# Performance work log

Measured on AMD Instinct MI355X. Metric: run time of the kernel, lower is better.

## Reference

```python
import jax, jax.numpy as jnp
import numpy as np

B, S, D, H, K = 2, 2048, 1024, 16, 16


def setup_inputs() -> dict:
    key = jax.random.key(0)
    ks = jax.random.split(key, 8)
    s = 0.02
    def w(k, shape):
        return s * jax.random.normal(k, shape, jnp.float32)
    return {
        "x": jax.random.normal(ks[0], (B, S, D), jnp.float32),
        "Wq": w(ks[1], (D, D)), "bq": jnp.zeros((D,), jnp.float32),
        "Wk": w(ks[2], (D, D)), "bk": jnp.zeros((D,), jnp.float32),
        "Wv": w(ks[3], (D, D)), "bv": jnp.zeros((D,), jnp.float32),
        "Wo": w(ks[4], (D, D)), "bo": jnp.zeros((D,), jnp.float32),
        "Ws1": w(ks[5], (D, D // 2)), "bs1": jnp.zeros((D // 2,), jnp.float32),
        "Ws2": w(ks[6], (D // 2, 1)), "bs2": jnp.zeros((1,), jnp.float32),
    }


def reference(x, Wq, bq, Wk, bk, Wv, bv, Wo, bo, Ws1, bs1, Ws2, bs2):
    Bx, Sx, Dx = x.shape
    Dh = Dx // H
    # QKV projections -> [B, H, S, Dh]
    q = (x @ Wq + bq).reshape(Bx, Sx, H, Dh).transpose(0, 2, 1, 3)
    k = (x @ Wk + bk).reshape(Bx, Sx, H, Dh).transpose(0, 2, 1, 3)
    v = (x @ Wv + bv).reshape(Bx, Sx, H, Dh).transpose(0, 2, 1, 3)
    scores = jnp.einsum('bhqd,bhkd->bhqk', q, k) / np.float32(np.sqrt(Dh))
    # Lightning-indexer importance: [B, S]; identical across heads, so compute once.
    imp = jax.nn.sigmoid(jax.nn.relu(x @ Ws1 + bs1) @ Ws2 + bs2)[..., 0]
    _, idx = jax.lax.top_k(imp, K)  # [B, K]
    sel = jnp.zeros((Bx, Sx), bool).at[jnp.arange(Bx)[:, None], idx].set(True)
    # sparse mask: position (i, j) kept if row i OR column j is a top-k token
    m2 = sel[:, :, None] | sel[:, None, :]  # [B, S, S]
    masked = jnp.where(m2[:, None, :, :], scores, -jnp.inf)
    w = jax.nn.softmax(masked, axis=-1)
    att = jnp.einsum('bhqk,bhkd->bhqd', w, v).transpose(0, 2, 1, 3).reshape(Bx, Sx, Dx)
    return att @ Wo + bo
```

## Files before the change

kernel.cpp:

```cpp
#include <hip/hip_runtime.h>
#include <math.h>

constexpr int Bb = 2, Ss = 2048, Dd = 1024, Hh = 16, Kk = 16;
constexpr float DELTA = 0.02f;

typedef __bf16 bf16x8 __attribute__((ext_vector_type(8)));
typedef __bf16 bf16x4 __attribute__((ext_vector_type(4)));
typedef float  f32x4  __attribute__((ext_vector_type(4)));

__device__ __forceinline__ void gld_lds16(const void* g, void* l) {
    __builtin_amdgcn_global_load_lds(
        (const __attribute__((address_space(1))) unsigned int*)g,
        (__attribute__((address_space(3))) unsigned int*)l, 16, 0, 0);
}

__global__ void __launch_bounds__(256) prep_kernel(
    const float* __restrict__ x, __bf16* __restrict__ xb,
    __bf16* __restrict__ xbT,
    float* __restrict__ imp, float* __restrict__ hbuf,
    float* __restrict__ qkvsel, int* __restrict__ ccount,
    const float* __restrict__ Ws1, __bf16* __restrict__ W1Th,
    const float* __restrict__ bv, const float* __restrict__ bo,
    float* __restrict__ Y, float* __restrict__ zbuf,
    float* __restrict__ obuf)
{
    __shared__ float tile[32][33];
    const int bid = blockIdx.x;
    const int t   = threadIdx.x;

    if (bid < 1024) {
        int i = bid * 256 + t;
        float4 z4 = {0.f, 0.f, 0.f, 0.f};
        if (i < 131072) ((float4*)Y)[i] = z4;
        if (i < 16384)  ((float4*)hbuf)[i] = z4;
        if (i < 24576)  ((float4*)qkvsel)[i] = z4;
        if (i < 8192)   ((float4*)zbuf)[i] = ((const float4*)bv)[i & 255];
        if (i < 8192)   ((float4*)obuf)[i] = ((const float4*)bo)[i & 255];
        if (i < 1024)   ((float4*)imp)[i] = z4;
        if (i < Bb)     ccount[i] = 0;
        return;
    }
    if (bid < 5120) {
        int tid = bid - 1024;
        int b   = tid >> 11;
        int rem = tid & 2047;
        int rt  = rem >> 5;
        int ct  = rem & 31;
        int tx = t & 31, ty = t >> 5;
        const float* xp = x + (size_t)b * Ss * Dd;
        __bf16* xbp = xb + (size_t)b * Ss * Dd;
        #pragma unroll
        for (int i2 = 0; i2 < 32; i2 += 8) {
            float v = xp[(size_t)(rt * 32 + ty + i2) * 1024 + ct * 32 + tx];
            tile[ty + i2][tx] = v;
            xbp[(size_t)(rt * 32 + ty + i2) * 1024 + ct * 32 + tx] = (__bf16)v;
        }
        __syncthreads();
        __bf16* xT = xbT + (size_t)b * Dd * Ss;
        #pragma unroll
        for (int i2 = 0; i2 < 32; i2 += 8)
            xT[(size_t)(ct * 32 + ty + i2) * 2048 + rt * 32 + tx] = (__bf16)tile[tx][ty + i2];
        return;
    }
    {
        int tid = bid - 5120;
        int n0 = (tid & 15) * 32;
        int k0 = (tid >> 4) * 32;
        int tx = t & 31, ty = t >> 5;
        #pragma unroll
        for (int i2 = 0; i2 < 32; i2 += 8)
            tile[ty + i2][tx] = Ws1[(size_t)(k0 + ty + i2) * 512 + n0 + tx];
        __syncthreads();
        #pragma unroll
        for (int i2 = 0; i2 < 32; i2 += 8)
            W1Th[(size_t)(n0 + ty + i2) * 1024 + k0 + tx] = (__bf16)tile[tx][ty + i2];
    }
}

__global__ void __launch_bounds__(256) gemm_ind(
    const __bf16* __restrict__ xb, const __bf16* __restrict__ W1Th,
    const float* __restrict__ bs1, const float* __restrict__ Ws2,
    float* __restrict__ imp)
{
    __shared__ __bf16 As[64 * 64];
    __shared__ __bf16 Bs[128 * 64];

    const int cb   = blockIdx.x;
    const int bm   = blockIdx.y * 64;
    const int t    = threadIdx.x;
    const int wave = t >> 6;
    const int lane = t & 63;
    const int wm   = (wave & 1) * 32;
    const int wn   = (wave >> 1) * 64;
    const int fr   = lane & 15;
    const int fq   = lane >> 4;
    const int K    = Dd;

    const __bf16* BT = W1Th + (size_t)cb * 128 * 1024;

    f32x4 acc[2][4] = {};

    for (int k0 = 0; k0 < K; k0 += 64) {
        #pragma unroll
        for (int l = 0; l < 2; ++l) {
            int c = l * 256 + t;
            int row = c >> 3, seg = (c & 7) ^ (row & 7);
            gld_lds16(xb + (size_t)(bm + row) * K + k0 + seg * 8,
                      As + (size_t)(l * 256 + wave * 64) * 8);
        }
        #pragma unroll
        for (int l = 0; l < 4; ++l) {
            int c = l * 256 + t;
            int row = c >> 3, seg = (c & 7) ^ (row & 7);
            gld_lds16(BT + (size_t)row * K + k0 + seg * 8,
                      Bs + (size_t)(l * 256 + wave * 64) * 8);
        }
        __syncthreads();
        #pragma unroll
        for (int s = 0; s < 2; ++s) {
            bf16x8 af[2], bf[4];
            #pragma unroll
            for (int i = 0; i < 2; ++i) {
                int row = wm + i * 16 + fr;
                af[i] = *(const bf16x8*)(As + row * 64 + (((s * 4 + fq) ^ (row & 7)) * 8));
            }
            #pragma unroll
            for (int j = 0; j < 4; ++j) {
                int row = wn + j * 16 + fr;
                bf[j] = *(const bf16x8*)(Bs + row * 64 + (((s * 4 + fq) ^ (row & 7)) * 8));
            }
            #pragma unroll
            for (int i = 0; i < 2; ++i)
                #pragma unroll
                for (int j = 0; j < 4; ++j)
                    acc[i][j] = __builtin_amdgcn_mfma_f32_16x16x32_bf16(af[i], bf[j], acc[i][j], 0, 0, 0);
        }
        __syncthreads();
    }

    const int cr = (lane >> 4) * 4;
    const int cc = lane & 15;
    float bb[4], w2[4];
    #pragma unroll
    for (int j = 0; j < 4; ++j) {
        int col = cb * 128 + wn + j * 16 + cc;
        bb[j] = bs1[col];
        w2[j] = Ws2[col];
    }
    #pragma unroll
    for (int i = 0; i < 2; ++i) {
        #pragma unroll
        for (int r = 0; r < 4; ++r) {
            float vsum = 0.f;
            #pragma unroll
            for (int j = 0; j < 4; ++j)
                vsum += fmaxf(acc[i][j][r] + bb[j], 0.f) * w2[j];
            #pragma unroll
            for (int off = 8; off > 0; off >>= 1)
                vsum += __shfl_xor(vsum, off, 16);
            if (cc == 0)
                atomicAdd(imp + (bm + wm + i * 16 + cr + r), vsum);
        }
    }
}

__global__ void __launch_bounds__(256) topk_fast(
    const float* __restrict__ imp, int* __restrict__ cand_idx,
    int* __restrict__ ccount)
{
    __shared__ float vals[2048];
    __shared__ float thr_s;
    __shared__ int   cnt_s;
    const int b = blockIdx.x;
    const int t = threadIdx.x;

    #pragma unroll
    for (int e = 0; e < 8; ++e)
        vals[t + 256 * e] = imp[b * Ss + t + 256 * e];
    __syncthreads();

    if (t < 64) {
        const int base = t * 32;
        for (int it = 0; it < Kk; ++it) {
            float best = -1e30f; int bidx = 0x7fffffff;
            #pragma unroll 8
            for (int j = 0; j < 32; ++j) {
                float v = vals[base + j];
                if (v > best) { best = v; bidx = base + j; }
            }
            #pragma unroll
            for (int off = 32; off > 0; off >>= 1) {
                float ov = __shfl_xor(best, off, 64);
                int   oi = __shfl_xor(bidx, off, 64);
                if (ov > best || (ov == best && oi < bidx)) { best = ov; bidx = oi; }
            }
            if (t == 0) {
                cand_idx[b * 64 + it] = bidx;
                vals[bidx] = -1e30f;
                if (it == Kk - 1) { thr_s = best - DELTA; cnt_s = Kk; }
            }
        }
    }
    __syncthreads();

    float thr = thr_s;
    #pragma unroll
    for (int e = 0; e < 8; ++e) {
        if (vals[t + 256 * e] > thr) {
            int p = atomicAdd(&cnt_s, 1);
            if (p < 64) cand_idx[b * 64 + p] = t + 256 * e;
        }
    }
    __syncthreads();
    if (t == 0) ccount[b] = min(cnt_s, 64);
}

__global__ void __launch_bounds__(256) rescore_h(
    const float* __restrict__ x, const float* __restrict__ Ws1,
    const int* __restrict__ cand_idx, const int* __restrict__ ccount,
    float* __restrict__ hbuf)
{
    const int c = blockIdx.x, kc = blockIdx.y, b = blockIdx.z;
    if (c >= ccount[b]) return;
    const int row = cand_idx[b * 64 + c];
    const int t = threadIdx.x;
    const int k0 = kc * 64;

    __shared__ float xs[64];
    if (t < 16)
        ((float4*)xs)[t] = ((const float4*)(x + ((size_t)(b * Ss + row)) * Dd + k0))[t];
    __syncthreads();

    float a0 = 0.f, a1 = 0.f;
    const float* W = Ws1 + (size_t)k0 * 512;
    #pragma unroll 16
    for (int kk = 0; kk < 64; ++kk) {
        float xv = xs[kk];
        a0 = fmaf(xv, W[kk * 512 + t], a0);
        a1 = fmaf(xv, W[kk * 512 + t + 256], a1);
    }
    float* hb = hbuf + ((size_t)(b * 64 + c)) * 512;
    atomicAdd(hb + t, a0);
    atomicAdd(hb + t + 256, a1);
}

__global__ void __launch_bounds__(256) rescore_fin_sel(
    const float* __restrict__ hbuf, const float* __restrict__ bs1,
    const float* __restrict__ Ws2, const int* __restrict__ cand_idx,
    const int* __restrict__ ccount, int* __restrict__ sel_idx)
{
    const int b = blockIdx.x;
    const int t = threadIdx.x;
    __shared__ float czv[64];
    __shared__ int   cidx[64];
    const int cntb = ccount[b];

    {
        const int cc = t >> 2, part = t & 3;
        const float* hb = hbuf + ((size_t)(b * 64 + cc)) * 512;
        float z = 0.f;
        const int j0 = part * 128;
        for (int j = j0; j < j0 + 128; ++j)
            z += fmaxf(hb[j] + bs1[j], 0.f) * Ws2[j];
        z += __shfl_xor(z, 1, 4);
        z += __shfl_xor(z, 2, 4);
        if (part == 0) { czv[cc] = z; cidx[cc] = cand_idx[b * 64 + cc]; }
    }
    __syncthreads();

    if (t < 64) {
        float val = (t < cntb) ? czv[t] : -1e30f;
        int   row = (t < cntb) ? cidx[t] : 0x7fffffff;
        for (int it = 0; it < Kk; ++it) {
            float bv = val; int br = row;
            #pragma unroll
            for (int off = 1; off < 64; off <<= 1) {
                float ov = __shfl_xor(bv, off, 64);
                int   orw = __shfl_xor(br, off, 64);
                if (ov > bv || (ov == bv && orw < br)) { bv = ov; br = orw; }
            }
            if (row == br) val = -1e30f;
            if (t == 0) sel_idx[b * Kk + it] = br;
        }
    }
}

__global__ void __launch_bounds__(256) proj_sel(
    const float* __restrict__ x,
    const float* __restrict__ Wq, const float* __restrict__ Wk,
    const float* __restrict__ Wv,
    const int* __restrict__ sel_idx, float* __restrict__ qkvsel)
{
    const int cx = blockIdx.x;
    const int m  = blockIdx.y;
    const int kc = blockIdx.z;
    const int t  = threadIdx.x;
    __shared__ int   sj[32];
    __shared__ float xs[32][128];

    if (t < 32) sj[t] = sel_idx[t];
    __syncthreads();

    const int k0 = kc * 128;
    #pragma unroll
    for (int l = 0; l < 4; ++l) {
        int c = l * 256 + t;
        int r = c >> 5, kq = c & 31;
        int b = r >> 4;
        float4 v = *(const float4*)(x + ((size_t)(b * Ss + sj[r])) * Dd + k0 + kq * 4);
        *(float4*)&xs[r][kq * 4] = v;
    }
    __syncthreads();

    const float* W = (m == 0) ? Wq : (m == 1) ? Wk : Wv;
    const int col = cx * 128 + (t & 127);
    const int rh  = t >> 7;
    float acc[16] = {};
    #pragma unroll 4
    for (int kk = 0; kk < 128; ++kk) {
        float wv = W[(size_t)(k0 + kk) * 1024 + col];
        #pragma unroll
        for (int r = 0; r < 16; ++r)
            acc[r] = fmaf(xs[rh * 16 + r][kk], wv, acc[r]);
    }
    #pragma unroll
    for (int r = 0; r < 16; ++r)
        atomicAdd(qkvsel + (size_t)(m * 32 + rh * 16 + r) * 1024 + col, acc[r]);
}

__global__ void __launch_bounds__(256) build_cdvo(
    const float* __restrict__ Wq, const float* __restrict__ Wk,
    const float* __restrict__ Wo,
    const float* __restrict__ bq, const float* __restrict__ bk,
    const float* __restrict__ bv,
    const float* __restrict__ qkvsel, float* __restrict__ beta,
    __bf16* __restrict__ ET, __bf16* __restrict__ VoT)
{
    const int nx = blockIdx.x;
    const int h  = blockIdx.y;
    const int b  = blockIdx.z;
    const int t  = threadIdx.x;
    __shared__ float qs[16][64], ks[16][64], vs[16][64];
    __shared__ float wt[128][65];

    #pragma unroll
    for (int l = 0; l < 12; ++l) {
        int c = l * 256 + t;
        int mat = c >> 10, rem = c & 1023;
        int row = rem >> 6, d = rem & 63;
        const float* bias = (mat == 0) ? bq : (mat == 1) ? bk : bv;
        float v = qkvsel[(size_t)(mat * 32 + b * 16 + row) * 1024 + h * 64 + d]
                + bias[h * 64 + d];
        if (mat == 0) qs[row][d] = v;
        else if (mat == 1) ks[row][d] = v;
        else vs[row][d] = v;
    }
    __syncthreads();

    if (nx == 0 && t < 16) {
        float a = 0.f;
        #pragma unroll 8
        for (int d = 0; d < 64; ++d) a = fmaf(bq[h * 64 + d], ks[t][d], a);
        beta[b * 256 + h * 16 + t] = a;
    }

    const int nl = t & 127;
    const int n  = nx * 128 + nl;
    const int sg = t >> 7;

    #pragma unroll
    for (int l = 0; l < 8; ++l) {
        int c = l * 256 + t;
        int rn = c >> 4, c4 = c & 15;
        float4 v = *(const float4*)(Wq + (size_t)(nx * 128 + rn) * 1024 + h * 64 + c4 * 4);
        wt[rn][c4 * 4 + 0] = v.x; wt[rn][c4 * 4 + 1] = v.y;
        wt[rn][c4 * 4 + 2] = v.z; wt[rn][c4 * 4 + 3] = v.w;
    }
    __syncthreads();
    {
        float acc[8] = {};
        #pragma unroll 8
        for (int d = 0; d < 64; ++d) {
            float wv = wt[nl][d];
            #pragma unroll
            for (int s = 0; s < 8; ++s)
                acc[s] = fmaf(wv, ks[sg * 8 + s][d], acc[s]);
        }
        #pragma unroll
        for (int s = 0; s < 8; ++s)
            ET[(size_t)(b * 512 + h * 16 + sg * 8 + s) * 1024 + n] = (__bf16)acc[s];
    }
    __syncthreads();

    #pragma unroll
    for (int l = 0; l < 8; ++l) {
        int c = l * 256 + t;
        int rn = c >> 4, c4 = c & 15;
        float4 v = *(const float4*)(Wk + (size_t)(nx * 128 + rn) * 1024 + h * 64 + c4 * 4);
        wt[rn][c4 * 4 + 0] = v.x; wt[rn][c4 * 4 + 1] = v.y;
        wt[rn][c4 * 4 + 2] = v.z; wt[rn][c4 * 4 + 3] = v.w;
    }
    __syncthreads();
    {
        float acc[8] = {};
        #pragma unroll 8
        for (int d = 0; d < 64; ++d) {
            float wv = wt[nl][d];
            #pragma unroll
            for (int s = 0; s < 8; ++s)
                acc[s] = fmaf(wv, qs[sg * 8 + s][d], acc[s]);
        }
        #pragma unroll
        for (int s = 0; s < 8; ++s)
            ET[(size_t)(b * 512 + 256 + h * 16 + sg * 8 + s) * 1024 + n] = (__bf16)acc[s];
    }

    {
        float acc[8] = {};
        #pragma unroll 8
        for (int d = 0; d < 64; ++d) {
            float wv = Wo[(size_t)(h * 64 + d) * 1024 + n];
            #pragma unroll
            for (int s = 0; s < 8; ++s)
                acc[s] = fmaf(wv, vs[sg * 8 + s][d], acc[s]);
        }
        #pragma unroll
        for (int s = 0; s < 8; ++s)
            VoT[((size_t)b * 1024 + n) * 256 + h * 16 + sg * 8 + s] = (__bf16)acc[s];
    }
}

__global__ void __launch_bounds__(256) gemm_scores(
    const __bf16* __restrict__ xb, const __bf16* __restrict__ ET,
    float* __restrict__ Ssp, float* __restrict__ SdT)
{
    __shared__ __bf16 As[64 * 64];
    __shared__ __bf16 Bs[128 * 64];

    const int b    = blockIdx.z;
    const int bn   = blockIdx.x * 128;
    const int bm   = blockIdx.y * 64;
    const int t    = threadIdx.x;
    const int wave = t >> 6;
    const int lane = t & 63;
    const int wm   = (wave & 1) * 32;
    const int wn   = (wave >> 1) * 64;
    const int fr   = lane & 15;
    const int fq   = lane >> 4;
    const int K    = Dd;

    const __bf16* A  = xb + (size_t)b * Ss * Dd;
    const __bf16* BT = ET + (size_t)b * 512 * 1024 + (size_t)bn * 1024;

    f32x4 acc[2][4] = {};

    for (int k0 = 0; k0 < K; k0 += 64) {
        #pragma unroll
        for (int l = 0; l < 2; ++l) {
            int c = l * 256 + t;
            int row = c >> 3, seg = (c & 7) ^ (row & 7);
            gld_lds16(A + (size_t)(bm + row) * K + k0 + seg * 8,
                      As + (size_t)(l * 256 + wave * 64) * 8);
        }
        #pragma unroll
        for (int l = 0; l < 4; ++l) {
            int c = l * 256 + t;
            int row = c >> 3, seg = (c & 7) ^ (row & 7);
            gld_lds16(BT + (size_t)row * K + k0 + seg * 8,
                      Bs + (size_t)(l * 256 + wave * 64) * 8);
        }
        __syncthreads();
        #pragma unroll
        for (int s = 0; s < 2; ++s) {
            bf16x8 af[2], bf[4];
            #pragma unroll
            for (int i = 0; i < 2; ++i) {
                int row = wm + i * 16 + fr;
                af[i] = *(const bf16x8*)(As + row * 64 + (((s * 4 + fq) ^ (row & 7)) * 8));
            }
            #pragma unroll
            for (int j = 0; j < 4; ++j) {
                int row = wn + j * 16 + fr;
                bf[j] = *(const bf16x8*)(Bs + row * 64 + (((s * 4 + fq) ^ (row & 7)) * 8));
            }
            #pragma unroll
            for (int i = 0; i < 2; ++i)
                #pragma unroll
                for (int j = 0; j < 4; ++j)
                    acc[i][j] = __builtin_amdgcn_mfma_f32_16x16x32_bf16(af[i], bf[j], acc[i][j], 0, 0, 0);
        }
        __syncthreads();
    }

    const int cr = (lane >> 4) * 4;
    const int cc = lane & 15;
    #pragma unroll
    for (int j = 0; j < 4; ++j) {
        int col = bn + wn + j * 16 + cc;
        #pragma unroll
        for (int i = 0; i < 2; ++i) {
            int row0 = bm + wm + i * 16 + cr;
            if (col < 256) {
                #pragma unroll
                for (int r = 0; r < 4; ++r)
                    Ssp[((size_t)b * 2048 + row0 + r) * 256 + col] = acc[i][j][r];
            } else {
                *(f32x4*)(SdT + ((size_t)b * 256 + col - 256) * 2048 + row0) = acc[i][j];
            }
        }
    }
}

__global__ void __launch_bounds__(256) sm_all(
    const float* __restrict__ Ssp, const float* __restrict__ beta,
    __bf16* __restrict__ Wsp,
    const float* __restrict__ SdT, __bf16* __restrict__ WdT)
{
    __shared__ float red[256];
    const int b = blockIdx.y;
    const int t = threadIdx.x;

    if (blockIdx.x < 512) {
        const int r = blockIdx.x * 4 + (t >> 6);
        const int l = t & 63;
        float4 v  = *(const float4*)(Ssp + ((size_t)b * 2048 + r) * 256 + l * 4);
        float4 bt = *(const float4*)(beta + b * 256 + l * 4);
        float e0 = __expf((v.x + bt.x) * 0.125f);
        float e1 = __expf((v.y + bt.y) * 0.125f);
        float e2 = __expf((v.z + bt.z) * 0.125f);
        float e3 = __expf((v.w + bt.w) * 0.125f);
        float ps = e0 + e1 + e2 + e3;
        ps += __shfl_xor(ps, 1, 64);
        ps += __shfl_xor(ps, 2, 64);
        float inv = 1.f / ps;
        bf16x4 w = { (__bf16)(e0 * inv), (__bf16)(e1 * inv),
                     (__bf16)(e2 * inv), (__bf16)(e3 * inv) };
        *(bf16x4*)(Wsp + ((size_t)b * 2048 + r) * 256 + l * 4) = w;
    } else {
        const int cx = blockIdx.x - 512;
        const float* Sp = SdT + ((size_t)b * 256 + cx) * 2048;
        float4 v0 = *(const float4*)(Sp + t * 8);
        float4 v1 = *(const float4*)(Sp + t * 8 + 4);
        float e[8];
        e[0] = __expf(v0.x * 0.125f); e[1] = __expf(v0.y * 0.125f);
        e[2] = __expf(v0.z * 0.125f); e[3] = __expf(v0.w * 0.125f);
        e[4] = __expf(v1.x * 0.125f); e[5] = __expf(v1.y * 0.125f);
        e[6] = __expf(v1.z * 0.125f); e[7] = __expf(v1.w * 0.125f);
        float ps = 0.f;
        #pragma unroll
        for (int i = 0; i < 8; ++i) ps += e[i];
        red[t] = ps;
        __syncthreads();
        for (int off = 128; off > 0; off >>= 1) {
            if (t < off) red[t] += red[t + off];
            __syncthreads();
        }
        float inv = 1.f / red[0];
        bf16x8 w;
        #pragma unroll
        for (int i = 0; i < 8; ++i) w[i] = (__bf16)(e[i] * inv);
        *(bf16x8*)(WdT + ((size_t)b * 256 + cx) * 2048 + t * 8) = w;
    }
}

__device__ __forceinline__ void gemm_bt_body(
    __bf16* As, __bf16* Bs,
    const __bf16* __restrict__ A, const __bf16* __restrict__ BT,
    const float* __restrict__ bias, float* __restrict__ C,
    int N, int K, int bm, int bn, int kc, int kchunks, int t)
{
    const int wave = t >> 6;
    const int lane = t & 63;
    const int wm   = (wave & 1) * 32;
    const int wn   = (wave >> 1) * 64;
    const int fr   = lane & 15;
    const int fq   = lane >> 4;
    const int KC   = K / kchunks;
    const int kend = (kc + 1) * KC;

    f32x4 acc[2][4] = {};

    for (int k0 = kc * KC; k0 < kend; k0 += 64) {
        #pragma unroll
        for (int l = 0; l < 2; ++l) {
            int c = l * 256 + t;
            int row = c >> 3, seg = (c & 7) ^ (row & 7);
            gld_lds16(A + (size_t)(bm + row) * K + k0 + seg * 8,
                      As + (size_t)(l * 256 + wave * 64) * 8);
        }
        #pragma unroll
        for (int l = 0; l < 4; ++l) {
            int c = l * 256 + t;
            int row = c >> 3, seg = (c & 7) ^ (row & 7);
            gld_lds16(BT + (size_t)(bn + row) * K + k0 + seg * 8,
                      Bs + (size_t)(l * 256 + wave * 64) * 8);
        }
        __syncthreads();
        #pragma unroll
        for (int s = 0; s < 2; ++s) {
            bf16x8 af[2], bf[4];
            #pragma unroll
            for (int i = 0; i < 2; ++i) {
                int row = wm + i * 16 + fr;
                af[i] = *(const bf16x8*)(As + row * 64 + (((s * 4 + fq) ^ (row & 7)) * 8));
            }
            #pragma unroll
            for (int j = 0; j < 4; ++j) {
                int row = wn + j * 16 + fr;
                bf[j] = *(const bf16x8*)(Bs + row * 64 + (((s * 4 + fq) ^ (row & 7)) * 8));
            }
            #pragma unroll
            for (int i = 0; i < 2; ++i)
                #pragma unroll
                for (int j = 0; j < 4; ++j)
                    acc[i][j] = __builtin_amdgcn_mfma_f32_16x16x32_bf16(af[i], bf[j], acc[i][j], 0, 0, 0);
        }
        __syncthreads();
    }

    const int cr = (lane >> 4) * 4;
    const int cc = lane & 15;
    #pragma unroll
    for (int j = 0; j < 4; ++j) {
        int col = bn + wn + j * 16 + cc;
        if (kchunks == 1) {
            float bb = bias ? bias[col] : 0.f;
            #pragma unroll
            for (int i = 0; i < 2; ++i)
                #pragma unroll
                for (int r = 0; r < 4; ++r)
                    C[(size_t)(bm + wm + i * 16 + cr + r) * N + col] = acc[i][j][r] + bb;
        } else {
            #pragma unroll
            for (int i = 0; i < 2; ++i)
                #pragma unroll
                for (int r = 0; r < 4; ++r)
                    atomicAdd(C + (size_t)(bm + wm + i * 16 + cr + r) * N + col, acc[i][j][r]);
        }
    }
}

__global__ void __launch_bounds__(256) gemm_bt2x(
    const __bf16* __restrict__ Wsp, const __bf16* __restrict__ VoT,
    const float* __restrict__ bo, float* __restrict__ out,
    const __bf16* __restrict__ WdT, const __bf16* __restrict__ xbT,
    float* __restrict__ Y)
{
    __shared__ __bf16 As[64 * 64];
    __shared__ __bf16 Bs[128 * 64];
    const int t = threadIdx.x;
    int id = blockIdx.x;
    if (id < 512) {
        int bx = id & 7, by = (id >> 3) & 31, bz = id >> 8;
        gemm_bt_body(As, Bs,
                     Wsp + (size_t)bz * 2048 * 256, VoT + (size_t)bz * 1024 * 256,
                     bo, out + (size_t)bz * 2048 * 1024,
                     1024, 256, by * 64, bx * 128, 0, 1, t);
    } else {
        id -= 512;
        int bx = id & 7, by = (id >> 3) & 3, z = id >> 5;
        int batch = z >> 1, kc = z & 1;
        gemm_bt_body(As, Bs,
                     WdT + (size_t)batch * 256 * 2048, xbT + (size_t)batch * 1024 * 2048,
                     nullptr, Y + (size_t)batch * 256 * 1024,
                     1024, 2048, by * 64, bx * 128, kc, 2, t);
    }
}

__global__ void __launch_bounds__(256) dense_z2(
    const float* __restrict__ Y, const float* __restrict__ Wv,
    float* __restrict__ zbuf)
{
    const int h = blockIdx.x, kc = blockIdx.y, b = blockIdx.z;
    const int t = threadIdx.x;
    __shared__ float Ys[16][128];
    const int k0 = kc * 128;
    #pragma unroll
    for (int l = 0; l < 2; ++l) {
        int c = l * 256 + t;
        int row = c >> 5, c4 = c & 31;
        *(float4*)&Ys[row][c4 * 4] =
            *(const float4*)(Y + ((size_t)(b * 256 + h * 16 + row)) * 1024 + k0 + c4 * 4);
    }
    __syncthreads();
    const int d = t & 63, tg = t >> 6;
    float acc[4] = {};
    #pragma unroll 8
    for (int kk = 0; kk < 128; ++kk) {
        float wv = Wv[(size_t)(k0 + kk) * 1024 + h * 64 + d];
        #pragma unroll
        for (int tt = 0; tt < 4; ++tt)
            acc[tt] = fmaf(Ys[tg * 4 + tt][kk], wv, acc[tt]);
    }
    #pragma unroll
    for (int tt = 0; tt < 4; ++tt)
        atomicAdd(zbuf + ((size_t)(b * 16 + tg * 4 + tt)) * 1024 + h * 64 + d, acc[tt]);
}

__global__ void __launch_bounds__(256) dense_out2(
    const float* __restrict__ zbuf, const float* __restrict__ Wo,
    float* __restrict__ obuf)
{
    const int nt = blockIdx.x, kc = blockIdx.y, b = blockIdx.z;
    const int t = threadIdx.x;
    __shared__ float zs[16][128];
    const int k0 = kc * 128;
    #pragma unroll
    for (int l = 0; l < 2; ++l) {
        int c = l * 256 + t;
        int row = c >> 5, c4 = c & 31;
        *(float4*)&zs[row][c4 * 4] =
            *(const float4*)(zbuf + ((size_t)(b * 16 + row)) * 1024 + k0 + c4 * 4);
    }
    __syncthreads();
    const int n = nt * 64 + (t & 63), tg = t >> 6;
    float acc[4] = {};
    #pragma unroll 8
    for (int kk = 0; kk < 128; ++kk) {
        float wv = Wo[(size_t)(k0 + kk) * 1024 + n];
        #pragma unroll
        for (int tt = 0; tt < 4; ++tt)
            acc[tt] = fmaf(zs[tg * 4 + tt][kk], wv, acc[tt]);
    }
    #pragma unroll
    for (int tt = 0; tt < 4; ++tt)
        atomicAdd(obuf + ((size_t)(b * 16 + tg * 4 + tt)) * 1024 + n, acc[tt]);
}

__global__ void __launch_bounds__(256) scatter_out(
    const float* __restrict__ obuf, const int* __restrict__ sel_idx,
    float* __restrict__ out)
{
    const int bid = blockIdx.x;
    const int b = bid >> 4, row = bid & 15;
    const int i = sel_idx[b * 16 + row];
    f32x4 v = *(const f32x4*)(obuf + ((size_t)(b * 16 + row)) * 1024 + threadIdx.x * 4);
    *(f32x4*)(out + ((size_t)(b * 2048 + i)) * 1024 + threadIdx.x * 4) = v;
}

extern "C" void kernel_launch(void* const* d_in, const int* in_sizes, int n_in,
                              void* d_out, int out_size, void* d_ws, size_t ws_size,
                              hipStream_t stream)
{
    const float* x   = (const float*)d_in[0];
    const float* Wq  = (const float*)d_in[1];
    const float* bq  = (const float*)d_in[2];
    const float* Wk  = (const float*)d_in[3];
    const float* bk  = (const float*)d_in[4];
    const float* Wv  = (const float*)d_in[5];
    const float* bv  = (const float*)d_in[6];
    const float* Wo  = (const float*)d_in[7];
    const float* bo  = (const float*)d_in[8];
    const float* Ws1 = (const float*)d_in[9];
    const float* bs1 = (const float*)d_in[10];
    const float* Ws2 = (const float*)d_in[11];
    float* out = (float*)d_out;

    const size_t MSD = (size_t)Bb * Ss * Dd;

    char* p = (char*)d_ws;
    __bf16* xb    = (__bf16*)p; p += MSD * sizeof(__bf16);
    __bf16* xbT   = (__bf16*)p; p += MSD * sizeof(__bf16);
    __bf16* W1Th  = (__bf16*)p; p += (size_t)512 * 1024 * sizeof(__bf16);
    __bf16* ET    = (__bf16*)p; p += (size_t)2 * 512 * 1024 * sizeof(__bf16);
    __bf16* VoT   = (__bf16*)p; p += (size_t)2 * 1024 * 256 * sizeof(__bf16);
    __bf16* Wsp   = (__bf16*)p; p += (size_t)2 * 2048 * 256 * sizeof(__bf16);
    __bf16* WdT   = (__bf16*)p; p += (size_t)2 * 256 * 2048 * sizeof(__bf16);
    float* Ssp    = (float*)p; p += (size_t)2 * 2048 * 256 * sizeof(float);
    float* SdT    = (float*)p; p += (size_t)2 * 256 * 2048 * sizeof(float);
    float* Y      = (float*)p; p += (size_t)2 * 256 * 1024 * sizeof(float);
    float* zbuf   = (float*)p; p += (size_t)2 * 16 * 1024 * sizeof(float);
    float* obuf   = (float*)p; p += (size_t)2 * 16 * 1024 * sizeof(float);
    float* imp    = (float*)p; p += (size_t)Bb * Ss * sizeof(float);
    float* hbuf   = (float*)p; p += (size_t)Bb * 64 * 512 * sizeof(float);
    float* qkvsel = (float*)p; p += (size_t)3 * 32 * 1024 * sizeof(float);
    float* beta   = (float*)p; p += (size_t)2 * 256 * sizeof(float);
    int* sel_idx  = (int*)p; p += (size_t)Bb * Kk * sizeof(int);
    int* cand_idx = (int*)p; p += (size_t)Bb * 64 * sizeof(int);
    int* ccount   = (int*)p; p += Bb * sizeof(int);

    prep_kernel<<<dim3(5632), 256, 0, stream>>>(
        x, xb, xbT, imp, hbuf, qkvsel, ccount, Ws1, W1Th,
        bv, bo, Y, zbuf, obuf);
    gemm_ind<<<dim3(4, 64), 256, 0, stream>>>(xb, W1Th, bs1, Ws2, imp);
    topk_fast<<<dim3(Bb), 256, 0, stream>>>(imp, cand_idx, ccount);
    rescore_h<<<dim3(64, 16, Bb), 256, 0, stream>>>(x, Ws1, cand_idx, ccount, hbuf);
    rescore_fin_sel<<<dim3(Bb), 256, 0, stream>>>(
        hbuf, bs1, Ws2, cand_idx, ccount, sel_idx);
    proj_sel<<<dim3(8, 3, 8), 256, 0, stream>>>(x, Wq, Wk, Wv, sel_idx, qkvsel);
    build_cdvo<<<dim3(8, 16, 2), 256, 0, stream>>>(
        Wq, Wk, Wo, bq, bk, bv, qkvsel, beta, ET, VoT);
    gemm_scores<<<dim3(4, 32, 2), 256, 0, stream>>>(xb, ET, Ssp, SdT);
    sm_all<<<dim3(768, 2), 256, 0, stream>>>(Ssp, beta, Wsp, SdT, WdT);
    gemm_bt2x<<<dim3(640), 256, 0, stream>>>(Wsp, VoT, bo, out, WdT, xbT, Y);
    dense_z2<<<dim3(16, 8, 2), 256, 0, stream>>>(Y, Wv, zbuf);
    dense_out2<<<dim3(16, 8, 2), 256, 0, stream>>>(zbuf, Wo, obuf);
    scatter_out<<<dim3(32), 256, 0, stream>>>(obuf, sel_idx, out);
}
```

Measured before the change: 256.8 us.

## Fuse sparse softmax into score GEMM epilogue and scatter into output GEMV

The per-head 16-column softmax for the selected-key scores now runs inside the gemm_scores epilogue, using 16-lane shuffles, and writes bf16 weights directly. This removes the fp32 Ssp intermediate and its read-back. The dense_out2 kernel now atomically adds straight into the selected output rows. Those rows are first reset to the bias in the gemm_bt2x epilogue, which removes the obuf buffer, its initialisation and the scatter_out launch. In exchange the epilogue does uncoalesced scalar bf16 stores and a 16-way compare per output element.

```diff
diff --git a/kernel.cpp b/kernel.cpp
--- a/kernel.cpp
+++ b/kernel.cpp
@@ -20,9 +20,8 @@
     float* __restrict__ imp, float* __restrict__ hbuf,
     float* __restrict__ qkvsel, int* __restrict__ ccount,
     const float* __restrict__ Ws1, __bf16* __restrict__ W1Th,
-    const float* __restrict__ bv, const float* __restrict__ bo,
-    float* __restrict__ Y, float* __restrict__ zbuf,
-    float* __restrict__ obuf)
+    const float* __restrict__ bv,
+    float* __restrict__ Y, float* __restrict__ zbuf)
 {
     __shared__ float tile[32][33];
     const int bid = blockIdx.x;
@@ -35,7 +34,6 @@
         if (i < 16384)  ((float4*)hbuf)[i] = z4;
         if (i < 24576)  ((float4*)qkvsel)[i] = z4;
         if (i < 8192)   ((float4*)zbuf)[i] = ((const float4*)bv)[i & 255];
-        if (i < 8192)   ((float4*)obuf)[i] = ((const float4*)bo)[i & 255];
         if (i < 1024)   ((float4*)imp)[i] = z4;
         if (i < Bb)     ccount[i] = 0;
         return;
@@ -432,7 +430,8 @@
 
 __global__ void __launch_bounds__(256) gemm_scores(
     const __bf16* __restrict__ xb, const __bf16* __restrict__ ET,
-    float* __restrict__ Ssp, float* __restrict__ SdT)
+    const float* __restrict__ beta, __bf16* __restrict__ Wsp,
+    float* __restrict__ SdT)
 {
     __shared__ __bf16 As[64 * 64];
     __shared__ __bf16 Bs[128 * 64];
@@ -494,80 +493,75 @@
 
     const int cr = (lane >> 4) * 4;
     const int cc = lane & 15;
-    #pragma unroll
-    for (int j = 0; j < 4; ++j) {
-        int col = bn + wn + j * 16 + cc;
-        #pragma unroll
-        for (int i = 0; i < 2; ++i) {
-            int row0 = bm + wm + i * 16 + cr;
-            if (col < 256) {
+    if (bn < 256) {
+        #pragma unroll
+        for (int j = 0; j < 4; ++j) {
+            int col = bn + wn + j * 16 + cc;
+            float bt = beta[b * 256 + col];
+            #pragma unroll
+            for (int i = 0; i < 2; ++i) {
                 #pragma unroll
-                for (int r = 0; r < 4; ++r)
-                    Ssp[((size_t)b * 2048 + row0 + r) * 256 + col] = acc[i][j][r];
-            } else {
+                for (int r = 0; r < 4; ++r) {
+                    float e = __expf((acc[i][j][r] + bt) * 0.125f);
+                    float ps = e;
+                    ps += __shfl_xor(ps, 1, 16);
+                    ps += __shfl_xor(ps, 2, 16);
+                    ps += __shfl_xor(ps, 4, 16);
+                    ps += __shfl_xor(ps, 8, 16);
+                    int row = bm + wm + i * 16 + cr + r;
+                    Wsp[((size_t)b * 2048 + row) * 256 + col] = (__bf16)(e / ps);
+                }
+            }
+        }
+    } else {
+        #pragma unroll
+        for (int j = 0; j < 4; ++j) {
+            int col = bn + wn + j * 16 + cc;
+            #pragma unroll
+            for (int i = 0; i < 2; ++i) {
+                int row0 = bm + wm + i * 16 + cr;
                 *(f32x4*)(SdT + ((size_t)b * 256 + col - 256) * 2048 + row0) = acc[i][j];
             }
         }
     }
 }
 
-__global__ void __launch_bounds__(256) sm_all(
-    const float* __restrict__ Ssp, const float* __restrict__ beta,
-    __bf16* __restrict__ Wsp,
+__global__ void __launch_bounds__(256) sm_dense(
     const float* __restrict__ SdT, __bf16* __restrict__ WdT)
 {
+    const int b = blockIdx.y, cx = blockIdx.x;
+    const int t = threadIdx.x;
     __shared__ float red[256];
-    const int b = blockIdx.y;
-    const int t = threadIdx.x;
-
-    if (blockIdx.x < 512) {
-        const int r = blockIdx.x * 4 + (t >> 6);
-        const int l = t & 63;
-        float4 v  = *(const float4*)(Ssp + ((size_t)b * 2048 + r) * 256 + l * 4);
-        float4 bt = *(const float4*)(beta + b * 256 + l * 4);
-        float e0 = __expf((v.x + bt.x) * 0.125f);
-        float e1 = __expf((v.y + bt.y) * 0.125f);
-        float e2 = __expf((v.z + bt.z) * 0.125f);
-        float e3 = __expf((v.w + bt.w) * 0.125f);
-        float ps = e0 + e1 + e2 + e3;
-        ps += __shfl_xor(ps, 1, 64);
-        ps += __shfl_xor(ps, 2, 64);
-        float inv = 1.f / ps;
-        bf16x4 w = { (__bf16)(e0 * inv), (__bf16)(e1 * inv),
-                     (__bf16)(e2 * inv), (__bf16)(e3 * inv) };
-        *(bf16x4*)(Wsp + ((size_t)b * 2048 + r) * 256 + l * 4) = w;
-    } else {
-        const int cx = blockIdx.x - 512;
-        const float* Sp = SdT + ((size_t)b * 256 + cx) * 2048;
-        float4 v0 = *(const float4*)(Sp + t * 8);
-        float4 v1 = *(const float4*)(Sp + t * 8 + 4);
-        float e[8];
-        e[0] = __expf(v0.x * 0.125f); e[1] = __expf(v0.y * 0.125f);
-        e[2] = __expf(v0.z * 0.125f); e[3] = __expf(v0.w * 0.125f);
-        e[4] = __expf(v1.x * 0.125f); e[5] = __expf(v1.y * 0.125f);
-        e[6] = __expf(v1.z * 0.125f); e[7] = __expf(v1.w * 0.125f);
-        float ps = 0.f;
-        #pragma unroll
-        for (int i = 0; i < 8; ++i) ps += e[i];
-        red[t] = ps;
-        __syncthreads();
-        for (int off = 128; off > 0; off >>= 1) {
-            if (t < off) red[t] += red[t + off];
-            __syncthreads();
-        }
-        float inv = 1.f / red[0];
-        bf16x8 w;
-        #pragma unroll
-        for (int i = 0; i < 8; ++i) w[i] = (__bf16)(e[i] * inv);
-        *(bf16x8*)(WdT + ((size_t)b * 256 + cx) * 2048 + t * 8) = w;
-    }
+    const float* Sp = SdT + ((size_t)b * 256 + cx) * 2048;
+    float4 v0 = *(const float4*)(Sp + t * 8);
+    float4 v1 = *(const float4*)(Sp + t * 8 + 4);
+    float e[8];
+    e[0] = __expf(v0.x * 0.125f); e[1] = __expf(v0.y * 0.125f);
+    e[2] = __expf(v0.z * 0.125f); e[3] = __expf(v0.w * 0.125f);
+    e[4] = __expf(v1.x * 0.125f); e[5] = __expf(v1.y * 0.125f);
+    e[6] = __expf(v1.z * 0.125f); e[7] = __expf(v1.w * 0.125f);
+    float ps = 0.f;
+    #pragma unroll
+    for (int i = 0; i < 8; ++i) ps += e[i];
+    red[t] = ps;
+    __syncthreads();
+    for (int off = 128; off > 0; off >>= 1) {
+        if (t < off) red[t] += red[t + off];
+        __syncthreads();
+    }
+    float inv = 1.f / red[0];
+    bf16x8 w;
+    #pragma unroll
+    for (int i = 0; i < 8; ++i) w[i] = (__bf16)(e[i] * inv);
+    *(bf16x8*)(WdT + ((size_t)b * 256 + cx) * 2048 + t * 8) = w;
 }
 
 __device__ __forceinline__ void gemm_bt_body(
     __bf16* As, __bf16* Bs,
     const __bf16* __restrict__ A, const __bf16* __restrict__ BT,
     const float* __restrict__ bias, float* __restrict__ C,
-    int N, int K, int bm, int bn, int kc, int kchunks, int t)
+    int N, int K, int bm, int bn, int kc, int kchunks, int t,
+    const int* sel16)
 {
     const int wave = t >> 6;
     const int lane = t & 63;
@@ -626,10 +620,20 @@
         if (kchunks == 1) {
             float bb = bias ? bias[col] : 0.f;
             #pragma unroll
-            for (int i = 0; i < 2; ++i)
+            for (int i = 0; i < 2; ++i) {
                 #pragma unroll
-                for (int r = 0; r < 4; ++r)
-                    C[(size_t)(bm + wm + i * 16 + cr + r) * N + col] = acc[i][j][r] + bb;
+                for (int r = 0; r < 4; ++r) {
+                    int row = bm + wm + i * 16 + cr + r;
+                    float v = acc[i][j][r] + bb;
+                    if (sel16) {
+                        bool issel = false;
+                        #pragma unroll
+                        for (int s2 = 0; s2 < 16; ++s2) issel |= (row == sel16[s2]);
+                        if (issel) v = bb;
+                    }
+                    C[(size_t)row * N + col] = v;
+                }
+            }
         } else {
             #pragma unroll
             for (int i = 0; i < 2; ++i)
@@ -644,18 +648,20 @@
     const __bf16* __restrict__ Wsp, const __bf16* __restrict__ VoT,
     const float* __restrict__ bo, float* __restrict__ out,
     const __bf16* __restrict__ WdT, const __bf16* __restrict__ xbT,
-    float* __restrict__ Y)
+    float* __restrict__ Y, const int* __restrict__ sel_idx)
 {
     __shared__ __bf16 As[64 * 64];
     __shared__ __bf16 Bs[128 * 64];
+    __shared__ int sjs[16];
     const int t = threadIdx.x;
     int id = blockIdx.x;
     if (id < 512) {
         int bx = id & 7, by = (id >> 3) & 31, bz = id >> 8;
+        if (t < 16) sjs[t] = sel_idx[bz * 16 + t];
         gemm_bt_body(As, Bs,
                      Wsp + (size_t)bz * 2048 * 256, VoT + (size_t)bz * 1024 * 256,
                      bo, out + (size_t)bz * 2048 * 1024,
-                     1024, 256, by * 64, bx * 128, 0, 1, t);
+                     1024, 256, by * 64, bx * 128, 0, 1, t, sjs);
     } else {
         id -= 512;
         int bx = id & 7, by = (id >> 3) & 3, z = id >> 5;
@@ -663,7 +669,7 @@
         gemm_bt_body(As, Bs,
                      WdT + (size_t)batch * 256 * 2048, xbT + (size_t)batch * 1024 * 2048,
                      nullptr, Y + (size_t)batch * 256 * 1024,
-                     1024, 2048, by * 64, bx * 128, kc, 2, t);
+                     1024, 2048, by * 64, bx * 128, kc, 2, t, nullptr);
     }
 }
 
@@ -699,11 +705,13 @@
 
 __global__ void __launch_bounds__(256) dense_out2(
     const float* __restrict__ zbuf, const float* __restrict__ Wo,
-    float* __restrict__ obuf)
+    const int* __restrict__ sel_idx, float* __restrict__ out)
 {
     const int nt = blockIdx.x, kc = blockIdx.y, b = blockIdx.z;
     const int t = threadIdx.x;
     __shared__ float zs[16][128];
+    __shared__ int sj[16];
+    if (t < 16) sj[t] = sel_idx[b * 16 + t];
     const int k0 = kc * 128;
     #pragma unroll
     for (int l = 0; l < 2; ++l) {
@@ -724,18 +732,7 @@
     }
     #pragma unroll
     for (int tt = 0; tt < 4; ++tt)
-        atomicAdd(obuf + ((size_t)(b * 16 + tg * 4 + tt)) * 1024 + n, acc[tt]);
-}
-
-__global__ void __launch_bounds__(256) scatter_out(
-    const float* __restrict__ obuf, const int* __restrict__ sel_idx,
-    float* __restrict__ out)
-{
-    const int bid = blockIdx.x;
-    const int b = bid >> 4, row = bid & 15;
-    const int i = sel_idx[b * 16 + row];
-    f32x4 v = *(const f32x4*)(obuf + ((size_t)(b * 16 + row)) * 1024 + threadIdx.x * 4);
-    *(f32x4*)(out + ((size_t)(b * 2048 + i)) * 1024 + threadIdx.x * 4) = v;
+        atomicAdd(out + ((size_t)(b * 2048 + sj[tg * 4 + tt])) * 1024 + n, acc[tt]);
 }
 
 extern "C" void kernel_launch(void* const* d_in, const int* in_sizes, int n_in,
@@ -766,11 +763,9 @@
     __bf16* VoT   = (__bf16*)p; p += (size_t)2 * 1024 * 256 * sizeof(__bf16);
     __bf16* Wsp   = (__bf16*)p; p += (size_t)2 * 2048 * 256 * sizeof(__bf16);
     __bf16* WdT   = (__bf16*)p; p += (size_t)2 * 256 * 2048 * sizeof(__bf16);
-    float* Ssp    = (float*)p; p += (size_t)2 * 2048 * 256 * sizeof(float);
     float* SdT    = (float*)p; p += (size_t)2 * 256 * 2048 * sizeof(float);
     float* Y      = (float*)p; p += (size_t)2 * 256 * 1024 * sizeof(float);
     float* zbuf   = (float*)p; p += (size_t)2 * 16 * 1024 * sizeof(float);
-    float* obuf   = (float*)p; p += (size_t)2 * 16 * 1024 * sizeof(float);
     float* imp    = (float*)p; p += (size_t)Bb * Ss * sizeof(float);
     float* hbuf   = (float*)p; p += (size_t)Bb * 64 * 512 * sizeof(float);
     float* qkvsel = (float*)p; p += (size_t)3 * 32 * 1024 * sizeof(float);
@@ -780,8 +775,7 @@
     int* ccount   = (int*)p; p += Bb * sizeof(int);
 
     prep_kernel<<<dim3(5632), 256, 0, stream>>>(
-        x, xb, xbT, imp, hbuf, qkvsel, ccount, Ws1, W1Th,
-        bv, bo, Y, zbuf, obuf);
+        x, xb, xbT, imp, hbuf, qkvsel, ccount, Ws1, W1Th, bv, Y, zbuf);
     gemm_ind<<<dim3(4, 64), 256, 0, stream>>>(xb, W1Th, bs1, Ws2, imp);
     topk_fast<<<dim3(Bb), 256, 0, stream>>>(imp, cand_idx, ccount);
     rescore_h<<<dim3(64, 16, Bb), 256, 0, stream>>>(x, Ws1, cand_idx, ccount, hbuf);
@@ -790,10 +784,10 @@
     proj_sel<<<dim3(8, 3, 8), 256, 0, stream>>>(x, Wq, Wk, Wv, sel_idx, qkvsel);
     build_cdvo<<<dim3(8, 16, 2), 256, 0, stream>>>(
         Wq, Wk, Wo, bq, bk, bv, qkvsel, beta, ET, VoT);
-    gemm_scores<<<dim3(4, 32, 2), 256, 0, stream>>>(xb, ET, Ssp, SdT);
-    sm_all<<<dim3(768, 2), 256, 0, stream>>>(Ssp, beta, Wsp, SdT, WdT);
-    gemm_bt2x<<<dim3(640), 256, 0, stream>>>(Wsp, VoT, bo, out, WdT, xbT, Y);
+    gemm_scores<<<dim3(4, 32, 2), 256, 0, stream>>>(xb, ET, beta, Wsp, SdT);
+    sm_dense<<<dim3(256, 2), 256, 0, stream>>>(SdT, WdT);
+    gemm_bt2x<<<dim3(640), 256, 0, stream>>>(
+        Wsp, VoT, bo, out, WdT, xbT, Y, sel_idx);
     dense_z2<<<dim3(16, 8, 2), 256, 0, stream>>>(Y, Wv, zbuf);
-    dense_out2<<<dim3(16, 8, 2), 256, 0, stream>>>(zbuf, Wo, obuf);
-    scatter_out<<<dim3(32), 256, 0, stream>>>(obuf, sel_idx, out);
-}
+    dense_out2<<<dim3(16, 8, 2), 256, 0, stream>>>(zbuf, Wo, sel_idx, out);
+}
```

New measurement: 261.9 us. About the same (+2.0%).
